# Kernel optimization log

Measured on AMD Instinct MI355X. Metric: run time of the kernel, lower is better.

## Reference

```python
import jax, jax.numpy as jnp
import numpy as np

P = 7          # corr_size (patch size)
PAD = P // 2   # displacement radius
PP = P * P     # 49 correlation channels
CHANS = [512, 1024, 512, 256, 256, 256]
HW = [64, 32, 16, 8, 4, 2]
B = 8


def _spatial_correlation(f1, f2):
    """out[b, pi*P+pj, y, x] = sum_c f1[b,c,y,x] * f2[b,c,y+pi-PAD, x+pj-PAD] (zero pad)."""
    Bb, C, H, W = f1.shape
    f2p = jnp.pad(f2, ((0, 0), (0, 0), (PAD, PAD), (PAD, PAD)))
    outs = [jnp.sum(f1 * f2p[:, :, di:di + H, dj:dj + W], axis=1)
            for di in range(P) for dj in range(P)]
    return jnp.stack(outs, axis=1)  # [B, P*P, H, W]


def _corr_lstm_cell(feat, feat_pre, h_pre, c_pre, w, b):
    corr = jax.nn.leaky_relu(_spatial_correlation(feat, feat_pre), 0.01)  # [B,49,H,W]
    lstm_in = jnp.concatenate([corr, h_pre], axis=1)                      # [B,98,H,W]
    conv = jax.lax.conv_general_dilated(
        lstm_in, w, window_strides=(1, 1), padding='SAME',
        dimension_numbers=('NCHW', 'OIHW', 'NCHW')) + b[None, :, None, None]
    cc_i, cc_f, cc_o, cc_g = jnp.split(conv, 4, axis=1)
    i = jax.nn.sigmoid(cc_i)
    f = jax.nn.sigmoid(cc_f)
    o = jax.nn.sigmoid(cc_o)
    g = jnp.tanh(cc_g)
    c_next = f * c_pre + i * g
    h_next = o * jnp.tanh(c_next)
    return h_next, c_next, corr


def setup_inputs() -> dict:
    key = jax.random.key(0)
    ks = jax.random.split(key, 6 * 6)
    d = {}
    ki = 0
    for l in range(6):
        C, S = CHANS[l], HW[l]
        d[f'x{l}'] = 0.05 * jax.random.normal(ks[ki], (B, C, S, S), jnp.float32); ki += 1
        d[f'xp{l}'] = 0.05 * jax.random.normal(ks[ki], (B, C, S, S), jnp.float32); ki += 1
        d[f'h{l}'] = 0.1 * jax.random.normal(ks[ki], (B, PP, S, S), jnp.float32); ki += 1
        d[f'c{l}'] = 0.1 * jax.random.normal(ks[ki], (B, PP, S, S), jnp.float32); ki += 1
        fan_in = 2 * PP * 9
        lim = float(np.sqrt(6.0 / (fan_in + 4 * PP * 9)))
        d[f'w{l}'] = jax.random.uniform(ks[ki], (4 * PP, 2 * PP, 3, 3), jnp.float32, -lim, lim); ki += 1
        bias = jnp.zeros((4 * PP,), jnp.float32).at[PP:2 * PP].set(1.0)  # forget-gate bias = 1
        d[f'b{l}'] = bias; ki += 1
    return d


def reference(x0, x1, x2, x3, x4, x5,
              xp0, xp1, xp2, xp3, xp4, xp5,
              h0, h1, h2, h3, h4, h5,
              c0, c1, c2, c3, c4, c5,
              w0, w1, w2, w3, w4, w5,
              b0, b1, b2, b3, b4, b5):
    xs = [x0, x1, x2, x3, x4, x5]
    xps = [xp0, xp1, xp2, xp3, xp4, xp5]
    hs = [h0, h1, h2, h3, h4, h5]
    cs = [c0, c1, c2, c3, c4, c5]
    ws = [w0, w1, w2, w3, w4, w5]
    bs = [b0, b1, b2, b3, b4, b5]
    outs = []
    for l in range(6):
        outs.append(_corr_lstm_cell(xs[l], xps[l], hs[l], cs[l], ws[l], bs[l]))
    h_next = tuple(o[0] for o in outs)
    c_next = tuple(o[1] for o in outs)
    corrs = tuple(o[2] for o in outs)
    return h_next + c_next + corrs  # flat 18-tuple
```

## Files before the change

### kernel.cpp

```cpp
#include <hip/hip_runtime.h>
#include <stdint.h>

#define DEV __device__ __forceinline__

typedef _Float16 half2_t __attribute__((ext_vector_type(2)));
typedef _Float16 half4_t __attribute__((ext_vector_type(4)));
typedef __bf16   bf16x8  __attribute__((ext_vector_type(8)));
typedef float    floatx4 __attribute__((ext_vector_type(4)));
typedef float    floatx2 __attribute__((ext_vector_type(2)));

DEV float fdot2f(half2_t a, half2_t b, float c) {
#if __has_builtin(__builtin_amdgcn_fdot2)
  return __builtin_amdgcn_fdot2(a, b, c, false);
#else
  return c + (float)a[0] * (float)b[0] + (float)a[1] * (float)b[1];
#endif
}

DEV half2_t pkh2(float a, float b) {
#if __has_builtin(__builtin_amdgcn_cvt_pkrtz)
  return __builtin_bit_cast(half2_t, __builtin_amdgcn_cvt_pkrtz(a, b));
#else
  half2_t r; r[0] = (_Float16)a; r[1] = (_Float16)b; return r;
#endif
}

DEV uint32_t f2bf(float f) {
  uint32_t u = __float_as_uint(f);
  return (u + 0x7FFFu + ((u >> 16) & 1u)) >> 16;
}

DEV void tile_barrier() {
  __builtin_amdgcn_sched_barrier(0);
  asm volatile("s_waitcnt lgkmcnt(0)" ::: "memory");
  __builtin_amdgcn_s_barrier();
  __builtin_amdgcn_sched_barrier(0);
}

struct CorrCfg {
  const float* gx[6]; const float* gxp[6];
  int wg_start[2];
  int mid_start;
  int small_start[3];
  int S[2], C[2], tiles_x[2], tiles_pb[2], cpl[2];
  int mcpl;
  int sS[3], sC[3], sNspl[3];
  long long poff[2], mpoff, spoff[3];
};

__global__ __launch_bounds__(256)
void corr_kernel(CorrCfg cfg, _Float16* __restrict__ partial)
{
  __shared__ half2_t ldsbuf[2][2][22*40] __attribute__((aligned(16)));
  const int tid = threadIdx.x;
  int wg = blockIdx.x;

  if (wg >= cfg.small_start[0]) {
    int lvl = (wg >= cfg.small_start[2]) ? 2 : (wg >= cfg.small_start[1]) ? 1 : 0;
    long long i = (long long)(wg - cfg.small_start[lvl])*256 + tid;
    const int S = cfg.sS[lvl], C = cfg.sC[lvl], SS = S*S;
    const int nsp = cfg.sNspl[lvl];
    const long long per = (long long)8*49*SS;
    if (i >= (long long)nsp*per) return;
    int sp = (int)(i / per);
    long long rem = i - (long long)sp*per;
    const int cpl = C / nsp, cbase = sp * cpl;
    const float* X  = cfg.gx[lvl+3];
    const float* XP = cfg.gxp[lvl+3];
    int xc_ = (int)(rem % S); int yc = (int)((rem/S) % S);
    int d = (int)((rem/SS) % 49); int b = (int)(rem/((long long)49*SS));
    int yy = yc + d/7 - 3, xx = xc_ + (d%7) - 3;
    float s = 0.f;
    if (yy >= 0 && yy < S && xx >= 0 && xx < S) {
      const float* xb = X  + ((size_t)b*C + cbase)*SS + (size_t)yc*S + xc_;
      const float* pb = XP + ((size_t)b*C + cbase)*SS + (size_t)yy*S + xx;
      #pragma unroll 8
      for (int c = 0; c < cpl; ++c) s += xb[(size_t)c*SS] * pb[(size_t)c*SS];
    }
    partial[cfg.spoff[lvl] + (long long)sp*per + rem] = (_Float16)s;
    return;
  }

  if (wg >= cfg.mid_start) {
    constexpr int NT = 256, MS = 16, MC = 512;
    constexpr int ROWS = 22, COLS = 22, ST = 23;
    constexpr int SLOTS = ROWS * 6 * 2;
    constexpr int PER = 2;
    int rel = wg - cfg.mid_start;
    const int cpl = cfg.mcpl;
    const int sp = rel >> 3;
    const int b = rel & 7;
    const int tx = tid & 15, ty = tid >> 4;
    const int cbase = sp * cpl;
    const size_t SS = (size_t)MS*MS;
    const float* Xb  = cfg.gx[2]  + (size_t)b*MC*SS;
    const float* XPb = cfg.gxp[2] + (size_t)b*MC*SS;
    const size_t qoff = (size_t)ty*MS + tx;

    int f_go[PER], f_base[PER], f_col0[PER], f_pr[PER];
    bool f_ok[PER], f_val[PER];
    #pragma unroll
    for (int s = 0; s < PER; ++s) {
      int i = tid + s*NT;
      bool val = (i < SLOTS);
      int ii = val ? i : 0;
      int pr = ii & 1;
      int rest = ii >> 1;
      int q = rest % 6;
      int r = rest / 6;
      int gy = r - 3;
      int gx0 = -4 + 4*q;
      bool ok = val && gy >= 0 && gy < MS && gx0 >= 0 && (gx0 + 3) < MS;
      f_val[s] = val; f_ok[s] = ok; f_pr[s] = pr;
      f_go[s] = ok ? gy*MS + gx0 : 0;
      f_col0[s] = 4*q - 1;
      f_base[s] = r*ST;
    }

    float acc[49];
    #pragma unroll
    for (int d = 0; d < 49; ++d) acc[d] = 0.f;
    floatx4 flA[PER][2], flB[PER][2], flC[PER][2];
    float xc[4], xn[4];

#define MFILL_LOAD(fl, c0v) { \
  _Pragma("unroll") for (int s = 0; s < PER; ++s) { \
    const float* p_ = XPb + (size_t)(cbase + (c0v) + 2*f_pr[s])*SS + f_go[s]; \
    if (f_ok[s]) { fl[s][0] = *(const floatx4*)p_; fl[s][1] = *(const floatx4*)(p_ + SS); } \
    else { fl[s][0] = (floatx4)0.f; fl[s][1] = (floatx4)0.f; } } }

#define MXLOAD(dst, c0v) { \
  _Pragma("unroll") for (int c = 0; c < 4; ++c) \
    dst[c] = Xb[(size_t)(cbase + (c0v) + c)*SS + qoff]; }

#define MFILL_STORE(bbv, fl) { \
  _Pragma("unroll") for (int s = 0; s < PER; ++s) if (f_val[s]) { \
    half2_t* plane_ = &ldsbuf[bbv][f_pr[s]][0]; \
    _Pragma("unroll") for (int j = 0; j < 4; ++j) { \
      int col_ = f_col0[s] + j; \
      if (col_ >= 0 && col_ < COLS) \
        plane_[f_base[s] + col_] = pkh2(fl[s][0][j], fl[s][1][j]); } } }

#define MCOMPUTE(bbv) { \
  _Pragma("unroll") for (int pr = 0; pr < 2; ++pr) { \
    half2_t xq = pkh2(xc[2*pr], xc[2*pr+1]); \
    _Pragma("unroll") for (int di = 0; di < 7; ++di) { \
      const half2_t* row_ = &ldsbuf[bbv][pr][(ty+di)*ST + tx]; \
      _Pragma("unroll") for (int dj = 0; dj < 7; ++dj) \
        acc[di*7+dj] = fdot2f(xq, row_[dj], acc[di*7+dj]); } } }

#define MXROT { _Pragma("unroll") for (int c = 0; c < 4; ++c) xc[c] = xn[c]; }

    const int nchunk = cpl >> 2;
    MFILL_LOAD(flA, 0); MXLOAD(xc, 0);
    MFILL_LOAD(flB, 4); MXLOAD(xn, 4);
    MFILL_STORE(0, flA);
    MFILL_LOAD(flC, 8);
    tile_barrier();
    for (int k = 0; k < nchunk; k += 3) {
      { const int bb = k & 1;
        if (k+1 < nchunk) MFILL_STORE(bb^1, flB);
        if (k+3 < nchunk) MFILL_LOAD(flA, (k+3)*4);
        MCOMPUTE(bb);
        MXROT;
        if (k+2 < nchunk) MXLOAD(xn, (k+2)*4);
        tile_barrier(); }
      if (k+1 < nchunk) { const int bb = (k+1) & 1;
        if (k+2 < nchunk) MFILL_STORE(bb^1, flC);
        if (k+4 < nchunk) MFILL_LOAD(flB, (k+4)*4);
        MCOMPUTE(bb);
        MXROT;
        if (k+3 < nchunk) MXLOAD(xn, (k+3)*4);
        tile_barrier(); }
      if (k+2 < nchunk) { const int bb = (k+2) & 1;
        if (k+3 < nchunk) MFILL_STORE(bb^1, flA);
        if (k+5 < nchunk) MFILL_LOAD(flC, (k+5)*4);
        MCOMPUTE(bb);
        MXROT;
        if (k+4 < nchunk) MXLOAD(xn, (k+4)*4);
        tile_barrier(); }
    }
#undef MFILL_LOAD
#undef MXLOAD
#undef MFILL_STORE
#undef MCOMPUTE
#undef MXROT

    _Float16* P = partial + cfg.mpoff + ((size_t)sp*8 + b)*49*SS + qoff;
    #pragma unroll
    for (int d = 0; d < 49; ++d) P[(size_t)d*SS] = (_Float16)acc[d];
    return;
  }

  {
    constexpr int NT = 256, TH = 16, TW = 32;
    constexpr int ROWS = TH + 6;
    constexpr int COLS = TW + 6;
    constexpr int QUADS = 10;
    constexpr int ST = TW + 8;
    constexpr int SLOTS = ROWS * QUADS * 2;
    constexpr int PER = 2;

    int lvl = (wg >= cfg.wg_start[1]) ? 1 : 0;
    wg -= cfg.wg_start[lvl];
    const float* X  = cfg.gx[lvl];
    const float* XP = cfg.gxp[lvl];
    const int S = cfg.S[lvl], C = cfg.C[lvl];
    const int txc = cfg.tiles_x[lvl], tpb = cfg.tiles_pb[lvl], cpl = cfg.cpl[lvl];
    const int per_split = 8 * tpb;
    const int sp = wg / per_split;
    const int rem = wg - sp*per_split;
    const int b = rem / tpb;
    const int t = rem - b*tpb;
    const int y0 = (t / txc) * TH, x0t = (t % txc) * TW;
    const int tx = tid & 15, ty = tid >> 4;
    const int cbase = sp * cpl;
    const size_t SS = (size_t)S*S;
    const float* Xb  = X  + (size_t)b*C*SS;
    const float* XPb = XP + (size_t)b*C*SS;
    const int py = y0 + ty, px = x0t + 2*tx;
    const size_t qoff = (size_t)py*S + px;

    int f_go[PER], f_base[PER], f_col0[PER], f_pr[PER];
    bool f_ok[PER], f_val[PER];
    #pragma unroll
    for (int s = 0; s < PER; ++s) {
      int i = tid + s*NT;
      bool val = (i < SLOTS);
      int ii = val ? i : 0;
      int pr = ii & 1;
      int rest = ii >> 1;
      int q = rest % QUADS;
      int r = rest / QUADS;
      int gy = y0 + r - 3;
      int gx0 = x0t - 4 + 4*q;
      bool ok = val && gy >= 0 && gy < S && gx0 >= 0 && (gx0 + 3) < S;
      f_val[s] = val; f_ok[s] = ok; f_pr[s] = pr;
      f_go[s] = ok ? gy*S + gx0 : 0;
      f_col0[s] = 4*q - 1;
      f_base[s] = r*ST;
    }

    floatx2 acc[49];
    #pragma unroll
    for (int d = 0; d < 49; ++d) acc[d] = (floatx2)0.f;
    floatx4 flA[PER][2], flB[PER][2], flC[PER][2];
    floatx2 xc[4], xn[4];

#define FILL_LOAD(fl, c0v) { \
  _Pragma("unroll") for (int s = 0; s < PER; ++s) { \
    const float* p_ = XPb + (size_t)(cbase + (c0v) + 2*f_pr[s])*SS + f_go[s]; \
    if (f_ok[s]) { fl[s][0] = *(const floatx4*)p_; fl[s][1] = *(const floatx4*)(p_ + SS); } \
    else { fl[s][0] = (floatx4)0.f; fl[s][1] = (floatx4)0.f; } } }

#define XLOAD(dst, c0v) { \
  _Pragma("unroll") for (int c = 0; c < 4; ++c) \
    dst[c] = *(const floatx2*)(Xb + (size_t)(cbase + (c0v) + c)*SS + qoff); }

#define FILL_STORE(bbv, fl) { \
  _Pragma("unroll") for (int s = 0; s < PER; ++s) if (f_val[s]) { \
    half2_t* plane_ = &ldsbuf[bbv][f_pr[s]][0]; \
    _Pragma("unroll") for (int j = 0; j < 4; ++j) { \
      int col_ = f_col0[s] + j; \
      if (col_ >= 0 && col_ < COLS) \
        plane_[f_base[s] + col_] = pkh2(fl[s][0][j], fl[s][1][j]); } } }

#define COMPUTE(bbv) { \
  _Pragma("unroll") for (int pr = 0; pr < 2; ++pr) { \
    half2_t xqa = pkh2(xc[2*pr].x, xc[2*pr+1].x); \
    half2_t xqb = pkh2(xc[2*pr].y, xc[2*pr+1].y); \
    _Pragma("unroll") for (int di = 0; di < 7; ++di) { \
      const half2_t* row_ = &ldsbuf[bbv][pr][(ty+di)*ST + 2*tx]; \
      half2_t L_[8]; \
      _Pragma("unroll") for (int k = 0; k < 4; ++k) { \
        half4_t v_ = *(const half4_t*)(row_ + 2*k); \
        L_[2*k]   = __builtin_shufflevector(v_, v_, 0, 1); \
        L_[2*k+1] = __builtin_shufflevector(v_, v_, 2, 3); } \
      _Pragma("unroll") for (int dj = 0; dj < 7; ++dj) { \
        acc[di*7+dj].x = fdot2f(xqa, L_[dj],   acc[di*7+dj].x); \
        acc[di*7+dj].y = fdot2f(xqb, L_[dj+1], acc[di*7+dj].y); } } } }

#define XROT { _Pragma("unroll") for (int c = 0; c < 4; ++c) xc[c] = xn[c]; }

    const int nchunk = cpl >> 2;
    FILL_LOAD(flA, 0); XLOAD(xc, 0);
    FILL_LOAD(flB, 4); XLOAD(xn, 4);
    FILL_STORE(0, flA);
    FILL_LOAD(flC, 8);
    tile_barrier();
    for (int k = 0; k < nchunk; k += 3) {
      { const int bb = k & 1;
        if (k+1 < nchunk) FILL_STORE(bb^1, flB);
        if (k+3 < nchunk) FILL_LOAD(flA, (k+3)*4);
        COMPUTE(bb);
        XROT;
        if (k+2 < nchunk) XLOAD(xn, (k+2)*4);
        tile_barrier(); }
      if (k+1 < nchunk) { const int bb = (k+1) & 1;
        if (k+2 < nchunk) FILL_STORE(bb^1, flC);
        if (k+4 < nchunk) FILL_LOAD(flB, (k+4)*4);
        COMPUTE(bb);
        XROT;
        if (k+3 < nchunk) XLOAD(xn, (k+3)*4);
        tile_barrier(); }
      if (k+2 < nchunk) { const int bb = (k+2) & 1;
        if (k+3 < nchunk) FILL_STORE(bb^1, flA);
        if (k+5 < nchunk) FILL_LOAD(flC, (k+5)*4);
        COMPUTE(bb);
        XROT;
        if (k+4 < nchunk) XLOAD(xn, (k+4)*4);
        tile_barrier(); }
    }
#undef FILL_LOAD
#undef XLOAD
#undef FILL_STORE
#undef COMPUTE
#undef XROT

    _Float16* P = partial + cfg.poff[lvl] + ((size_t)sp*8 + b)*49*SS + qoff;
    #pragma unroll
    for (int d = 0; d < 49; ++d) {
      half2_t pko = pkh2(acc[d].x, acc[d].y);
      *(uint32_t*)(P + (size_t)d*SS) = *(const uint32_t*)&pko;
    }
  }
}

__global__ __launch_bounds__(256)
void pack_w_kernel(const float* __restrict__ w0, const float* __restrict__ w1,
                   const float* __restrict__ w2, const float* __restrict__ w3,
                   const float* __restrict__ w4, const float* __restrict__ w5,
                   uint16_t* __restrict__ wpack)
{
  int idx = blockIdx.x*256 + threadIdx.x;
  int lvl = idx / 258048;
  int e = idx - lvl*258048;
  const float* W = lvl==0?w0:lvl==1?w1:lvl==2?w2:lvl==3?w3:lvl==4?w4:w5;
  int j = e & 7, lane = (e >> 3) & 63, rest = e >> 9;
  int s = rest % 36, tt = rest / 36;
  int n  = tt*16 + (lane & 15);
  int ch = (s & 3)*32 + (lane >> 4)*8 + j;
  int tap = s >> 2, ky = tap/3, kx = tap - 3*ky;
  float v = 0.f;
  if (n < 196 && ch < 98) v = W[((n*98 + ch)*3 + ky)*3 + kx];
  wpack[idx] = (uint16_t)f2bf(v);
}

struct P2Cfg {
  int blk_start[7];
  int S[6], nsplit[6], pxg[6], lg[6], gpb[6];
  long long poff[6], lstm_off[6], corr_off[6];
  const float* h[6];
};
__global__ __launch_bounds__(256)
void pass2_kernel(P2Cfg cfg, const _Float16* __restrict__ partial,
                  uint32_t* __restrict__ lstm, float* __restrict__ dout)
{
  __shared__ float lds[64*99];
  int blk = blockIdx.x;
  int lvl = 0;
  while (lvl < 5 && blk >= cfg.blk_start[lvl+1]) ++lvl;
  int rel = blk - cfg.blk_start[lvl];
  const int S = cfg.S[lvl], Sp = S + 2, SS = S*S;
  const int PXG = cfg.pxg[lvl], lg = cfg.lg[lvl], gpb = cfg.gpb[lvl];
  const int b = rel / gpb, g = rel - b*gpb;
  const int pixbase = g * PXG;
  const int tid = threadIdx.x;
  const int nsp = cfg.nsplit[lvl];
  const size_t spstride = (size_t)8*49*SS;
  for (int e = tid; e < PXG*98; e += 256) {
    int pxl = e & (PXG-1);
    int ch  = e >> lg;
    int pix = pixbase + pxl;
    float v;
    if (ch < 49) {
      const _Float16* P = partial + cfg.poff[lvl] + ((size_t)b*49 + ch)*SS + pix;
      float s = 0.f;
      for (int sp = 0; sp < nsp; ++sp) s += (float)P[(size_t)sp*spstride];
      s = s < 0.f ? 0.01f*s : s;
      dout[cfg.corr_off[lvl] + ((size_t)b*49 + ch)*SS + pix] = s;
      v = s;
    } else {
      v = cfg.h[lvl][((size_t)b*49 + (ch - 49))*SS + pix];
    }
    lds[pxl*99 + ch] = v;
  }
  __syncthreads();
  uint32_t* Lb = lstm + (cfg.lstm_off[lvl] >> 1);
  for (int f = tid; f < (PXG << 6); f += 256) {
    int pxl = f >> 6, c2 = f & 63;
    int pix = pixbase + pxl;
    int y = pix / S, x = pix - y*S;
    int c0 = 2*c2, c1 = c0 + 1;
    float v0 = c0 < 98 ? lds[pxl*99 + c0] : 0.f;
    float v1 = c1 < 98 ? lds[pxl*99 + c1] : 0.f;
    Lb[((size_t)(b*Sp + y + 1)*Sp + (x + 1))*64 + c2] = f2bf(v0) | (f2bf(v1) << 16);
  }
}

struct CCfg {
  int wg_start[7];
  int S[6], tiles_x[6], tiles_pb[6], lwsh[6], mfc[6], mgrp[6];
  long long lstm_off[6], wp_off[6], h_off[6], c_off[6];
  const float* cpre[6]; const float* bias[6];
};
__global__ __launch_bounds__(256)
void conv_kernel(CCfg cfg, const uint16_t* __restrict__ lstm,
                 const uint16_t* __restrict__ wpack, float* __restrict__ dout)
{
  __shared__ float gl[224*69];
  int wg = blockIdx.x;
  int lvl = 0;
  while (lvl < 5 && wg >= cfg.wg_start[lvl+1]) ++lvl;
  wg -= cfg.wg_start[lvl];
  const int S = cfg.S[lvl], Sp = S + 2;
  const int lwsh = cfg.lwsh[lvl], msk = (1 << lwsh) - 1;
  const int tpb = cfg.tiles_pb[lvl];
  const int b = wg / tpb, t = wg - b*tpb;
  const int ty0 = (t / cfg.tiles_x[lvl]) << (6 - lwsh);
  const int tx0 = (t % cfg.tiles_x[lvl]) << lwsh;
  const int tid = threadIdx.x;
  const int wave = tid >> 6, lane = tid & 63;
  const int nhalf = wave & 1, mhalf = wave >> 1;
  const int mfc = cfg.mfc[lvl];
  const bool active = (mhalf < cfg.mgrp[lvl]);
  const int mi = lane & 15, q = lane >> 4;
  const int SS = S*S;

  if (active) {
    const uint16_t* lb = lstm + cfg.lstm_off[lvl] + (size_t)b*Sp*Sp*128;
    int aoff[2];
    #pragma unroll
    for (int mf = 0; mf < 2; ++mf) {
      int p = mhalf*32 + mf*16 + mi;
      int pc = p < SS ? p : 0;
      int y = ty0 + (pc >> lwsh), xx = tx0 + (pc & msk);
      aoff[mf] = (y*Sp + xx)*128 + q*8;
    }
    const uint16_t* wb = wpack + cfg.wp_off[lvl]
                       + (size_t)(nhalf*7)*36*512 + (size_t)lane*8;
    floatx4 acc[2][7];
    #pragma unroll
    for (int mf = 0; mf < 2; ++mf)
      #pragma unroll
      for (int nt = 0; nt < 7; ++nt) acc[mf][nt] = (floatx4)0.0f;

#define CONV_LOAD(sv, AV, BV) { \
  int tap_ = (sv) >> 2, cs_ = (sv) & 3; \
  int ky_ = tap_ / 3, kx_ = tap_ - 3*ky_; \
  int ao_ = ((ky_*Sp + kx_) << 7) + (cs_ << 5); \
  _Pragma("unroll") for (int mf = 0; mf < 2; ++mf) \
    if (mf < mfc) AV[mf] = *(const bf16x8*)(lb + aoff[mf] + ao_); \
  _Pragma("unroll") for (int nt = 0; nt < 7; ++nt) \
    BV[nt] = *(const bf16x8*)(wb + (size_t)((nt)*36 + (sv))*512); }

#define CONV_MFMA(AV, BV) { \
  _Pragma("unroll") for (int nt = 0; nt < 7; ++nt) \
    _Pragma("unroll") for (int mf = 0; mf < 2; ++mf) \
      if (mf < mfc) acc[mf][nt] = __builtin_amdgcn_mfma_f32_16x16x32_bf16( \
                        AV[mf], BV[nt], acc[mf][nt], 0, 0, 0); }

    bf16x8 av0[2], bv0[7], av1[2], bv1[7];
    CONV_LOAD(0, av0, bv0);
    for (int s = 0; s < 36; s += 2) {
      CONV_LOAD(s+1, av1, bv1);
      CONV_MFMA(av0, bv0);
      if (s+2 < 36) CONV_LOAD(s+2, av0, bv0);
      CONV_MFMA(av1, bv1);
    }
#undef CONV_LOAD
#undef CONV_MFMA

    #pragma unroll
    for (int mf = 0; mf < 2; ++mf) {
      if (mf < mfc) {
        #pragma unroll
        for (int nt = 0; nt < 7; ++nt) {
          const int n = nhalf*112 + nt*16 + mi;
          if (n < 196) {
            #pragma unroll
            for (int r = 0; r < 4; ++r) {
              const int p = mhalf*32 + mf*16 + q*4 + r;
              gl[n*69 + p] = acc[mf][nt][r];
            }
          }
        }
      }
    }
  }
  __syncthreads();

  const int p2 = lane;
  const int grp = wave;
  if (p2 < SS) {
    const int y = ty0 + (p2 >> lwsh), xx = tx0 + (p2 & msk);
    const int pix = y*S + xx;
    const float* bb2 = cfg.bias[lvl];
    const float* cp  = cfg.cpre[lvl];
    const int ch0 = grp*13, chend = (grp == 3) ? 49 : grp*13 + 13;
    for (int ch = ch0; ch < chend; ++ch) {
      float ci  = gl[ch*69 + p2]        + bb2[ch];
      float cf  = gl[(ch+49)*69 + p2]   + bb2[ch+49];
      float co_ = gl[(ch+98)*69 + p2]   + bb2[ch+98];
      float cg  = gl[(ch+147)*69 + p2]  + bb2[ch+147];
      float ig = 1.f/(1.f + __expf(-ci));
      float fg = 1.f/(1.f + __expf(-cf));
      float og = 1.f/(1.f + __expf(-co_));
      float g  = 1.f - 2.f/(__expf(2.f*cg) + 1.f);
      size_t e = ((size_t)b*49 + ch)*SS + pix;
      float cpv = cp[e];
      float cn = fg*cpv + ig*g;
      float hn = og * (1.f - 2.f/(__expf(2.f*cn) + 1.f));
      dout[cfg.h_off[lvl] + e] = hn;
      dout[cfg.c_off[lvl] + e] = cn;
    }
  }
}

extern "C" void kernel_launch(void* const* d_in, const int* in_sizes, int n_in,
                              void* d_out, int out_size, void* d_ws, size_t ws_size,
                              hipStream_t stream)
{
  const float *x[6], *xp[6], *h[6], *cpre[6], *w[6], *bias[6];
  for (int l = 0; l < 6; ++l) {
    x[l]    = (const float*)d_in[6*l + 0];
    xp[l]   = (const float*)d_in[6*l + 1];
    h[l]    = (const float*)d_in[6*l + 2];
    cpre[l] = (const float*)d_in[6*l + 3];
    w[l]    = (const float*)d_in[6*l + 4];
    bias[l] = (const float*)d_in[6*l + 5];
  }
  static const int SL[6] = {64,32,16,8,4,2};
  static const int CL[6] = {512,1024,512,256,256,256};
  int NSPL[6] = {8,16,16,1,1,1};

  long long hsz[6], lstm_off[6], h_off[6], poff[6];
  long long a1 = 0, a3 = 0;
  for (int l = 0; l < 6; ++l) {
    int S = SL[l], Sp = S + 2;
    hsz[l] = 8LL*49*S*S;
    lstm_off[l] = a1; a1 += 8LL*Sp*Sp*128;
    h_off[l]    = a3; a3 += hsz[l];
  }
  long long pa = 0;
  for (int l = 0; l < 6; ++l) { poff[l] = pa; pa += (long long)NSPL[l]*hsz[l]; }
  {
    long long need = a1*2 + 6LL*258048*2 + pa*2;
    if (need > (long long)ws_size) {
      NSPL[0] = 4; NSPL[1] = 8; NSPL[2] = 16;
      pa = 0;
      for (int l = 0; l < 6; ++l) { poff[l] = pa; pa += (long long)NSPL[l]*hsz[l]; }
    }
  }
  const long long GRP = a3;
  const long long LSTM_ELEMS = a1;

  uint16_t* lstm  = (uint16_t*)d_ws;
  uint16_t* wpack = (uint16_t*)((char*)d_ws + LSTM_ELEMS*2);
  _Float16* partial = (_Float16*)((char*)d_ws + LSTM_ELEMS*2 + 6LL*258048*2);
  float* dout = (float*)d_out;

  {
    CorrCfg ccfg;
    static const int tpb2[2] = {8, 2};
    static const int txx2[2] = {2, 1};
    for (int l = 0; l < 6; ++l) { ccfg.gx[l] = x[l]; ccfg.gxp[l] = xp[l]; }
    int start = 0;
    for (int l = 0; l < 2; ++l) {
      ccfg.wg_start[l] = start;
      ccfg.S[l] = SL[l]; ccfg.C[l] = CL[l];
      ccfg.tiles_x[l] = txx2[l]; ccfg.tiles_pb[l] = tpb2[l];
      ccfg.cpl[l] = CL[l]/NSPL[l];
      ccfg.poff[l] = poff[l];
      start += NSPL[l]*8*tpb2[l];
    }
    ccfg.mid_start = start;
    ccfg.mcpl = CL[2]/NSPL[2];
    ccfg.mpoff = poff[2];
    start += NSPL[2]*8;
    for (int l = 0; l < 3; ++l) {
      ccfg.small_start[l] = start;
      ccfg.sS[l] = SL[l+3]; ccfg.sC[l] = CL[l+3];
      ccfg.sNspl[l] = NSPL[l+3];
      ccfg.spoff[l] = poff[l+3];
      start += (int)((NSPL[l+3]*hsz[l+3] + 255)/256);
    }
    corr_kernel<<<start, 256, 0, stream>>>(ccfg, partial);
  }
  (void)hipMemsetAsync(lstm, 0, (size_t)LSTM_ELEMS*2, stream);
  pack_w_kernel<<<6048, 256, 0, stream>>>(w[0],w[1],w[2],w[3],w[4],w[5], wpack);
  {
    P2Cfg p2; int start = 0;
    static const int PXGL[6] = {64,64,64,64,16,4};
    static const int LGL[6]  = {6,6,6,6,4,2};
    for (int l = 0; l < 6; ++l) {
      p2.blk_start[l] = start;
      int gpb = (SL[l]*SL[l]) / PXGL[l]; if (gpb < 1) gpb = 1;
      p2.gpb[l] = gpb;
      start += 8 * gpb;
      p2.S[l] = SL[l]; p2.nsplit[l] = NSPL[l];
      p2.pxg[l] = PXGL[l]; p2.lg[l] = LGL[l];
      p2.poff[l] = poff[l]; p2.lstm_off[l] = lstm_off[l];
      p2.corr_off[l] = 2*GRP + h_off[l];
      p2.h[l] = h[l];
    }
    p2.blk_start[6] = start;
    pass2_kernel<<<start, 256, 0, stream>>>(p2, partial, (uint32_t*)lstm, dout);
  }
  {
    CCfg cc;
    static const int ctpb[6] = {64, 16, 4, 1, 1, 1};
    static const int ctx[6]  = {4, 2, 1, 1, 1, 1};
    static const int clw[6]  = {4, 4, 4, 3, 2, 1};
    static const int cmfc[6] = {2, 2, 2, 2, 1, 1};
    static const int cmg[6]  = {2, 2, 2, 2, 1, 1};
    int start = 0;
    for (int l = 0; l < 6; ++l) {
      cc.wg_start[l] = start; start += 8*ctpb[l];
      cc.S[l] = SL[l]; cc.tiles_x[l] = ctx[l]; cc.tiles_pb[l] = ctpb[l];
      cc.lwsh[l] = clw[l]; cc.mfc[l] = cmfc[l]; cc.mgrp[l] = cmg[l];
      cc.lstm_off[l] = lstm_off[l];
      cc.wp_off[l] = 258048LL*l;
      cc.h_off[l] = h_off[l];
      cc.c_off[l] = GRP + h_off[l];
      cc.cpre[l] = cpre[l];
      cc.bias[l] = bias[l];
    }
    cc.wg_start[6] = start;
    conv_kernel<<<start, 256, 0, stream>>>(cc, lstm, wpack, dout);
  }
  (void)in_sizes; (void)n_in; (void)out_size; (void)ws_size;
}
```

Measured before the change: 518.0 us.

## Pack prefetched fills to fp16 at load time and shorten prefetch pipeline

Prefetched previous-frame tiles and current-frame vectors are now converted to packed half2 as soon as they are loaded, rather than held as float4 registers until the LDS store. The three-stage register rotation (flA/flB/flC plus an xc/xn copy) becomes a two-stage double-buffered loop with fixed LDS buffer indices. The aim is lower register pressure and fewer moves, which could allow higher occupancy. In exchange, loads run at a shallower prefetch distance, and converting right after the load forces a wait on that load earlier, which can expose memory latency.

```diff
diff --git a/kernel.cpp b/kernel.cpp
--- a/kernel.cpp
+++ b/kernel.cpp
@@ -120,71 +120,65 @@
     float acc[49];
     #pragma unroll
     for (int d = 0; d < 49; ++d) acc[d] = 0.f;
-    floatx4 flA[PER][2], flB[PER][2], flC[PER][2];
-    float xc[4], xn[4];
-
-#define MFILL_LOAD(fl, c0v) { \
+    half2_t pk[PER][4];
+    half2_t xq0[2], xq1[2];
+
+#define MFILL_LOADPK(c0v) { \
   _Pragma("unroll") for (int s = 0; s < PER; ++s) { \
     const float* p_ = XPb + (size_t)(cbase + (c0v) + 2*f_pr[s])*SS + f_go[s]; \
-    if (f_ok[s]) { fl[s][0] = *(const floatx4*)p_; fl[s][1] = *(const floatx4*)(p_ + SS); } \
-    else { fl[s][0] = (floatx4)0.f; fl[s][1] = (floatx4)0.f; } } }
-
-#define MXLOAD(dst, c0v) { \
-  _Pragma("unroll") for (int c = 0; c < 4; ++c) \
-    dst[c] = Xb[(size_t)(cbase + (c0v) + c)*SS + qoff]; }
-
-#define MFILL_STORE(bbv, fl) { \
+    floatx4 a_ = (floatx4)0.f, b2_ = (floatx4)0.f; \
+    if (f_ok[s]) { a_ = *(const floatx4*)p_; b2_ = *(const floatx4*)(p_ + SS); } \
+    _Pragma("unroll") for (int j = 0; j < 4; ++j) \
+      pk[s][j] = pkh2(a_[j], b2_[j]); } }
+
+#define MXLOADPK(dst, c0v) { \
+  float t0_ = Xb[(size_t)(cbase + (c0v) + 0)*SS + qoff]; \
+  float t1_ = Xb[(size_t)(cbase + (c0v) + 1)*SS + qoff]; \
+  float t2_ = Xb[(size_t)(cbase + (c0v) + 2)*SS + qoff]; \
+  float t3_ = Xb[(size_t)(cbase + (c0v) + 3)*SS + qoff]; \
+  dst[0] = pkh2(t0_, t1_); dst[1] = pkh2(t2_, t3_); }
+
+#define MFILL_STORE(bbv) { \
   _Pragma("unroll") for (int s = 0; s < PER; ++s) if (f_val[s]) { \
     half2_t* plane_ = &ldsbuf[bbv][f_pr[s]][0]; \
     _Pragma("unroll") for (int j = 0; j < 4; ++j) { \
       int col_ = f_col0[s] + j; \
       if (col_ >= 0 && col_ < COLS) \
-        plane_[f_base[s] + col_] = pkh2(fl[s][0][j], fl[s][1][j]); } } }
-
-#define MCOMPUTE(bbv) { \
+        plane_[f_base[s] + col_] = pk[s][j]; } } }
+
+#define MCOMPUTE(bbv, xq) { \
   _Pragma("unroll") for (int pr = 0; pr < 2; ++pr) { \
-    half2_t xq = pkh2(xc[2*pr], xc[2*pr+1]); \
+    half2_t xv = xq[pr]; \
     _Pragma("unroll") for (int di = 0; di < 7; ++di) { \
       const half2_t* row_ = &ldsbuf[bbv][pr][(ty+di)*ST + tx]; \
       _Pragma("unroll") for (int dj = 0; dj < 7; ++dj) \
-        acc[di*7+dj] = fdot2f(xq, row_[dj], acc[di*7+dj]); } } }
-
-#define MXROT { _Pragma("unroll") for (int c = 0; c < 4; ++c) xc[c] = xn[c]; }
+        acc[di*7+dj] = fdot2f(xv, row_[dj], acc[di*7+dj]); } } }
 
     const int nchunk = cpl >> 2;
-    MFILL_LOAD(flA, 0); MXLOAD(xc, 0);
-    MFILL_LOAD(flB, 4); MXLOAD(xn, 4);
-    MFILL_STORE(0, flA);
-    MFILL_LOAD(flC, 8);
+    MFILL_LOADPK(0); MXLOADPK(xq0, 0);
+    MFILL_STORE(0);
+    MFILL_LOADPK(4); MXLOADPK(xq1, 4);
     tile_barrier();
-    for (int k = 0; k < nchunk; k += 3) {
-      { const int bb = k & 1;
-        if (k+1 < nchunk) MFILL_STORE(bb^1, flB);
-        if (k+3 < nchunk) MFILL_LOAD(flA, (k+3)*4);
-        MCOMPUTE(bb);
-        MXROT;
-        if (k+2 < nchunk) MXLOAD(xn, (k+2)*4);
-        tile_barrier(); }
-      if (k+1 < nchunk) { const int bb = (k+1) & 1;
-        if (k+2 < nchunk) MFILL_STORE(bb^1, flC);
-        if (k+4 < nchunk) MFILL_LOAD(flB, (k+4)*4);
-        MCOMPUTE(bb);
-        MXROT;
-        if (k+3 < nchunk) MXLOAD(xn, (k+3)*4);
-        tile_barrier(); }
-      if (k+2 < nchunk) { const int bb = (k+2) & 1;
-        if (k+3 < nchunk) MFILL_STORE(bb^1, flA);
-        if (k+5 < nchunk) MFILL_LOAD(flC, (k+5)*4);
-        MCOMPUTE(bb);
-        MXROT;
-        if (k+4 < nchunk) MXLOAD(xn, (k+4)*4);
-        tile_barrier(); }
-    }
-#undef MFILL_LOAD
-#undef MXLOAD
+    for (int k = 0; k < nchunk; k += 2) {
+      {
+        if (k+1 < nchunk) MFILL_STORE(1);
+        if (k+2 < nchunk) MFILL_LOADPK((k+2)*4);
+        MCOMPUTE(0, xq0);
+        if (k+2 < nchunk) MXLOADPK(xq0, (k+2)*4);
+        tile_barrier();
+      }
+      if (k+1 < nchunk) {
+        if (k+2 < nchunk) MFILL_STORE(0);
+        if (k+3 < nchunk) MFILL_LOADPK((k+3)*4);
+        MCOMPUTE(1, xq1);
+        if (k+3 < nchunk) MXLOADPK(xq1, (k+3)*4);
+        tile_barrier();
+      }
+    }
+#undef MFILL_LOADPK
+#undef MXLOADPK
 #undef MFILL_STORE
 #undef MCOMPUTE
-#undef MXROT
 
     _Float16* P = partial + cfg.mpoff + ((size_t)sp*8 + b)*49*SS + qoff;
     #pragma unroll
@@ -244,31 +238,36 @@
     floatx2 acc[49];
     #pragma unroll
     for (int d = 0; d < 49; ++d) acc[d] = (floatx2)0.f;
-    floatx4 flA[PER][2], flB[PER][2], flC[PER][2];
-    floatx2 xc[4], xn[4];
-
-#define FILL_LOAD(fl, c0v) { \
+    half2_t pk[PER][4];
+    half2_t xq0[4], xq1[4];
+
+#define FILL_LOADPK(c0v) { \
   _Pragma("unroll") for (int s = 0; s < PER; ++s) { \
     const float* p_ = XPb + (size_t)(cbase + (c0v) + 2*f_pr[s])*SS + f_go[s]; \
-    if (f_ok[s]) { fl[s][0] = *(const floatx4*)p_; fl[s][1] = *(const floatx4*)(p_ + SS); } \
-    else { fl[s][0] = (floatx4)0.f; fl[s][1] = (floatx4)0.f; } } }
-
-#define XLOAD(dst, c0v) { \
-  _Pragma("unroll") for (int c = 0; c < 4; ++c) \
-    dst[c] = *(const floatx2*)(Xb + (size_t)(cbase + (c0v) + c)*SS + qoff); }
-
-#define FILL_STORE(bbv, fl) { \
+    floatx4 a_ = (floatx4)0.f, b2_ = (floatx4)0.f; \
+    if (f_ok[s]) { a_ = *(const floatx4*)p_; b2_ = *(const floatx4*)(p_ + SS); } \
+    _Pragma("unroll") for (int j = 0; j < 4; ++j) \
+      pk[s][j] = pkh2(a_[j], b2_[j]); } }
+
+#define XLOADPK(dst, c0v) { \
+  floatx2 t0_ = *(const floatx2*)(Xb + (size_t)(cbase + (c0v) + 0)*SS + qoff); \
+  floatx2 t1_ = *(const floatx2*)(Xb + (size_t)(cbase + (c0v) + 1)*SS + qoff); \
+  floatx2 t2_ = *(const floatx2*)(Xb + (size_t)(cbase + (c0v) + 2)*SS + qoff); \
+  floatx2 t3_ = *(const floatx2*)(Xb + (size_t)(cbase + (c0v) + 3)*SS + qoff); \
+  dst[0] = pkh2(t0_.x, t1_.x); dst[1] = pkh2(t0_.y, t1_.y); \
+  dst[2] = pkh2(t2_.x, t3_.x); dst[3] = pkh2(t2_.y, t3_.y); }
+
+#define FILL_STORE(bbv) { \
   _Pragma("unroll") for (int s = 0; s < PER; ++s) if (f_val[s]) { \
     half2_t* plane_ = &ldsbuf[bbv][f_pr[s]][0]; \
     _Pragma("unroll") for (int j = 0; j < 4; ++j) { \
       int col_ = f_col0[s] + j; \
       if (col_ >= 0 && col_ < COLS) \
-        plane_[f_base[s] + col_] = pkh2(fl[s][0][j], fl[s][1][j]); } } }
-
-#define COMPUTE(bbv) { \
+        plane_[f_base[s] + col_] = pk[s][j]; } } }
+
+#define COMPUTE(bbv, xq) { \
   _Pragma("unroll") for (int pr = 0; pr < 2; ++pr) { \
-    half2_t xqa = pkh2(xc[2*pr].x, xc[2*pr+1].x); \
-    half2_t xqb = pkh2(xc[2*pr].y, xc[2*pr+1].y); \
+    half2_t xqa = xq[2*pr], xqb = xq[2*pr+1]; \
     _Pragma("unroll") for (int di = 0; di < 7; ++di) { \
       const half2_t* row_ = &ldsbuf[bbv][pr][(ty+di)*ST + 2*tx]; \
       half2_t L_[8]; \
@@ -280,42 +279,31 @@
         acc[di*7+dj].x = fdot2f(xqa, L_[dj],   acc[di*7+dj].x); \
         acc[di*7+dj].y = fdot2f(xqb, L_[dj+1], acc[di*7+dj].y); } } } }
 
-#define XROT { _Pragma("unroll") for (int c = 0; c < 4; ++c) xc[c] = xn[c]; }
-
     const int nchunk = cpl >> 2;
-    FILL_LOAD(flA, 0); XLOAD(xc, 0);
-    FILL_LOAD(flB, 4); XLOAD(xn, 4);
-    FILL_STORE(0, flA);
-    FILL_LOAD(flC, 8);
+    FILL_LOADPK(0); XLOADPK(xq0, 0);
+    FILL_STORE(0);
+    FILL_LOADPK(4); XLOADPK(xq1, 4);
     tile_barrier();
-    for (int k = 0; k < nchunk; k += 3) {
-      { const int bb = k & 1;
-        if (k+1 < nchunk) FILL_STORE(bb^1, flB);
-        if (k+3 < nchunk) FILL_LOAD(flA, (k+3)*4);
-        COMPUTE(bb);
-        XROT;
-        if (k+2 < nchunk) XLOAD(xn, (k+2)*4);
-        tile_barrier(); }
-      if (k+1 < nchunk) { const int bb = (k+1) & 1;
-        if (k+2 < nchunk) FILL_STORE(bb^1, flC);
-        if (k+4 < nchunk) FILL_LOAD(flB, (k+4)*4);
-        COMPUTE(bb);
-        XROT;
-        if (k+3 < nchunk) XLOAD(xn, (k+3)*4);
-        tile_barrier(); }
-      if (k+2 < nchunk) { const int bb = (k+2) & 1;
-        if (k+3 < nchunk) FILL_STORE(bb^1, flA);
-        if (k+5 < nchunk) FILL_LOAD(flC, (k+5)*4);
-        COMPUTE(bb);
-        XROT;
-        if (k+4 < nchunk) XLOAD(xn, (k+4)*4);
-        tile_barrier(); }
-    }
-#undef FILL_LOAD
-#undef XLOAD
+    for (int k = 0; k < nchunk; k += 2) {
+      {
+        if (k+1 < nchunk) FILL_STORE(1);
+        if (k+2 < nchunk) FILL_LOADPK((k+2)*4);
+        COMPUTE(0, xq0);
+        if (k+2 < nchunk) XLOADPK(xq0, (k+2)*4);
+        tile_barrier();
+      }
+      if (k+1 < nchunk) {
+        if (k+2 < nchunk) FILL_STORE(0);
+        if (k+3 < nchunk) FILL_LOADPK((k+3)*4);
+        COMPUTE(1, xq1);
+        if (k+3 < nchunk) XLOADPK(xq1, (k+3)*4);
+        tile_barrier();
+      }
+    }
+#undef FILL_LOADPK
+#undef XLOADPK
 #undef FILL_STORE
 #undef COMPUTE
-#undef XROT
 
     _Float16* P = partial + cfg.poff[lvl] + ((size_t)sp*8 + b)*49*SS + qoff;
     #pragma unroll
```

New measurement: 469.2 us. -9.4%, faster.
